# Performance work log

Measured on AMD Instinct MI355X. Metric: run time of the kernel, lower is better.

Reference implementation:

```python
import jax, jax.numpy as jnp
import numpy as np
import hashlib

B, L, D, STEPS, VOCAB = 4, 8192, 2048, 8, 50257


def _sha256_c(tid: int):
    # Same hashing as FractalEmbedding._token_to_c_batch
    h = hashlib.sha256(str(int(tid)).encode()).hexdigest()
    real = int(h[:16], 16) / 2**64 - 0.5
    imag = int(h[16:32], 16) / 2**64 - 0.5
    return (real * 2.0, imag * 2.0)


def setup_inputs() -> dict:
    key = jax.random.key(0)
    k1, k2 = jax.random.split(key)
    token_ids = jax.random.randint(k1, (B, L), 0, VOCAB, dtype=jnp.int64)
    # sha256 is host-side, non-differentiable integer hashing: precompute the
    # per-token Julia constant c (faithful to _token_to_c_batch). Hash only the
    # unique ids, then gather.
    ids = np.asarray(token_ids)
    uniq, inv = np.unique(ids, return_inverse=True)
    cs_u = np.array([_sha256_c(t) for t in uniq], dtype=np.float32)  # [U,2]
    cs = jnp.asarray(cs_u[inv].reshape(B, L, 2))                      # [B,L,2]
    # nn.Linear(2*steps, embed_dim, bias=False) weight: [D, 2*steps]
    W = jax.random.normal(k2, (D, 2 * STEPS), dtype=jnp.float32) / np.sqrt(2 * STEPS)
    scale = jnp.ones((), dtype=jnp.float32)
    return {"token_ids": token_ids, "cs": cs, "W": W, "scale": scale}


def reference(token_ids, cs, W, scale):
    # Julia iteration z <- z^2 + c starting from z=0, recording (zr, zi)
    # interleaved at every step -> feats [B,L,2*steps].
    steps = W.shape[1] // 2
    cr, ci = cs[..., 0], cs[..., 1]
    zr = jnp.zeros_like(cr)
    zi = jnp.zeros_like(ci)
    vals = []
    for _ in range(steps):  # steps=8, tiny static loop
        zr, zi = zr * zr - zi * zi + cr, 2.0 * zr * zi + ci
        vals.append(zr)
        vals.append(zi)
    feats = jnp.stack(vals, axis=-1)  # [B,L,2*steps], interleaved re/im
    # out = proj(feats) * scale, proj has no bias
    return jnp.einsum('blf,df->bld', feats, W) * scale
```

## Files before the change

kernel.cpp:

```cpp
#include <hip/hip_runtime.h>


#define STEPS 8
#define KF 16
#define DDIM 2048
#define BLOCK 256
#define CPT 8
#define ROWS_PER_BLK 32

typedef float f32x2 __attribute__((ext_vector_type(2)));
typedef float f32x4 __attribute__((ext_vector_type(4)));

__global__ __launch_bounds__(BLOCK, 2) void fractal_embed_kernel(
    const float* __restrict__ cs,
    const float* __restrict__ W,
    const float* __restrict__ scale,
    float* __restrict__ out)
{
    const int tid  = threadIdx.x;
    const int row0 = blockIdx.x * ROWS_PER_BLK;
    const int ca   = tid * 4;
    const int cb   = 1024 + tid * 4;

    __shared__ float s_cs[2 * ROWS_PER_BLK];
    if (tid < 2 * ROWS_PER_BLK)
        s_cs[tid] = cs[(size_t)row0 * 2 + tid];

    const float s = scale[0];

    f32x2 w2[CPT][KF / 2];
#pragma unroll
    for (int r = 0; r < CPT; ++r) {
        const int d = (r < 4) ? (ca + r) : (cb + (r - 4));
        const f32x2* wp = reinterpret_cast<const f32x2*>(W + (size_t)d * KF);
#pragma unroll
        for (int q = 0; q < KF / 2; ++q) {
            f32x2 v = wp[q];
            v.x *= s; v.y *= s;
            w2[r][q] = v;
        }
    }
    __syncthreads();

#pragma unroll 2
    for (int rr = 0; rr < ROWS_PER_BLK; ++rr) {
        const int row = row0 + rr;
        const float cr = s_cs[2 * rr];
        const float ci = s_cs[2 * rr + 1];

        f32x2 f2[STEPS];
        float zr = 0.0f, zi = 0.0f;
#pragma unroll
        for (int st = 0; st < STEPS; ++st) {
            const float nzr = fmaf(zr, zr, fmaf(-zi, zi, cr));
            const float nzi = fmaf(zr + zr, zi, ci);
            zr = nzr; zi = nzi;
            f2[st].x = zr;
            f2[st].y = zi;
        }

        f32x4 oa, ob;
#pragma unroll
        for (int r = 0; r < CPT; ++r) {
            f32x2 a2 = {0.0f, 0.0f};
#pragma unroll
            for (int q = 0; q < KF / 2; ++q)
                a2 = __builtin_elementwise_fma(f2[q], w2[r][q], a2);
            const float v = a2.x + a2.y;
            if (r < 4) oa[r] = v;
            else       ob[r - 4] = v;
        }

        float* rowp = out + (size_t)row * DDIM;
        reinterpret_cast<f32x4*>(rowp + ca)[0] = oa;
        reinterpret_cast<f32x4*>(rowp + cb)[0] = ob;
    }
}

extern "C" void kernel_launch(void* const* d_in, const int* in_sizes, int n_in,
                              void* d_out, int out_size, void* d_ws, size_t ws_size,
                              hipStream_t stream) {
    const float* cs    = (const float*)d_in[1];
    const float* W     = (const float*)d_in[2];
    const float* scale = (const float*)d_in[3];
    float* out         = (float*)d_out;

    const int M = in_sizes[0];
    const int grid = M / ROWS_PER_BLK;
    fractal_embed_kernel<<<grid, BLOCK, 0, stream>>>(cs, W, scale, out);
}
```

Measured before the change: 57.00 us.

## Use persistent grid with grid-stride rows and 4 columns per thread

Replaces the per-block 32-row tiling with a fixed 1024-block persistent grid where each thread owns 4 contiguous columns and strides over rows in steps of 512. This halves per-thread W registers to allow higher occupancy, removes shared memory and the barrier, and prefetches the next row's Julia constant. The goal is better sustained store bandwidth on a write-bound kernel. Each thread now recomputes the Julia iteration for each row it visits, with fewer columns to amortize it over.

```diff
diff --git a/kernel.cpp b/kernel.cpp
--- a/kernel.cpp
+++ b/kernel.cpp
@@ -5,34 +5,29 @@
 #define KF 16
 #define DDIM 2048
 #define BLOCK 256
-#define CPT 8
-#define ROWS_PER_BLK 32
+#define GRID 1024
+#define ROWS_PER_STEP 512
 
 typedef float f32x2 __attribute__((ext_vector_type(2)));
 typedef float f32x4 __attribute__((ext_vector_type(4)));
 
-__global__ __launch_bounds__(BLOCK, 2) void fractal_embed_kernel(
+__global__ __launch_bounds__(BLOCK, 4) void fractal_embed_kernel(
     const float* __restrict__ cs,
     const float* __restrict__ W,
     const float* __restrict__ scale,
-    float* __restrict__ out)
+    float* __restrict__ out,
+    int iters)
 {
-    const int tid  = threadIdx.x;
-    const int row0 = blockIdx.x * ROWS_PER_BLK;
-    const int ca   = tid * 4;
-    const int cb   = 1024 + tid * 4;
-
-    __shared__ float s_cs[2 * ROWS_PER_BLK];
-    if (tid < 2 * ROWS_PER_BLK)
-        s_cs[tid] = cs[(size_t)row0 * 2 + tid];
+    const int g    = blockIdx.x * BLOCK + threadIdx.x;
+    const int col  = (4 * g) & (DDIM - 1);
+    const int row0 = (4 * g) >> 11;
 
     const float s = scale[0];
 
-    f32x2 w2[CPT][KF / 2];
+    f32x2 w2[4][KF / 2];
 #pragma unroll
-    for (int r = 0; r < CPT; ++r) {
-        const int d = (r < 4) ? (ca + r) : (cb + (r - 4));
-        const f32x2* wp = reinterpret_cast<const f32x2*>(W + (size_t)d * KF);
+    for (int r = 0; r < 4; ++r) {
+        const f32x2* wp = reinterpret_cast<const f32x2*>(W + (size_t)(col + r) * KF);
 #pragma unroll
         for (int q = 0; q < KF / 2; ++q) {
             f32x2 v = wp[q];
@@ -40,40 +35,39 @@
             w2[r][q] = v;
         }
     }
-    __syncthreads();
 
-#pragma unroll 2
-    for (int rr = 0; rr < ROWS_PER_BLK; ++rr) {
-        const int row = row0 + rr;
-        const float cr = s_cs[2 * rr];
-        const float ci = s_cs[2 * rr + 1];
+    const f32x2* cs2 = reinterpret_cast<const f32x2*>(cs);
+    f32x2 c = cs2[row0];
+
+#pragma unroll 1
+    for (int k = 0; k < iters; ++k) {
+        const int row = row0 + k * ROWS_PER_STEP;
+        f32x2 cn = c;
+        if (k + 1 < iters) cn = cs2[row + ROWS_PER_STEP];
 
         f32x2 f2[STEPS];
         float zr = 0.0f, zi = 0.0f;
 #pragma unroll
         for (int st = 0; st < STEPS; ++st) {
-            const float nzr = fmaf(zr, zr, fmaf(-zi, zi, cr));
-            const float nzi = fmaf(zr + zr, zi, ci);
+            const float nzr = fmaf(zr, zr, fmaf(-zi, zi, c.x));
+            const float nzi = fmaf(zr + zr, zi, c.y);
             zr = nzr; zi = nzi;
             f2[st].x = zr;
             f2[st].y = zi;
         }
 
-        f32x4 oa, ob;
+        f32x4 o;
 #pragma unroll
-        for (int r = 0; r < CPT; ++r) {
+        for (int r = 0; r < 4; ++r) {
             f32x2 a2 = {0.0f, 0.0f};
 #pragma unroll
             for (int q = 0; q < KF / 2; ++q)
                 a2 = __builtin_elementwise_fma(f2[q], w2[r][q], a2);
-            const float v = a2.x + a2.y;
-            if (r < 4) oa[r] = v;
-            else       ob[r - 4] = v;
+            o[r] = a2.x + a2.y;
         }
 
-        float* rowp = out + (size_t)row * DDIM;
-        reinterpret_cast<f32x4*>(rowp + ca)[0] = oa;
-        reinterpret_cast<f32x4*>(rowp + cb)[0] = ob;
+        reinterpret_cast<f32x4*>(out + (size_t)row * DDIM + col)[0] = o;
+        c = cn;
     }
 }
 
@@ -86,6 +80,6 @@
     float* out         = (float*)d_out;
 
     const int M = in_sizes[0];
-    const int grid = M / ROWS_PER_BLK;
-    fractal_embed_kernel<<<grid, BLOCK, 0, stream>>>(cs, W, scale, out);
+    const int iters = M / ROWS_PER_STEP;
+    fractal_embed_kernel<<<GRID, BLOCK, 0, stream>>>(cs, W, scale, out, iters);
 }
```

Result: slower. 68.51 us (+20.2%).
